# Kernel tuning notes

Measured on AMD Instinct MI355X. Metric: run time of the kernel, lower is better.

Reference implementation:

```python
import jax, jax.numpy as jnp
import numpy as np

U = 128  # linear_units

def setup_inputs() -> dict:
    key = jax.random.key(0)
    k1, k2, k3, k4, k5, k6 = jax.random.split(key, 6)
    B, S, D = 16, 2048, 128
    x = jax.random.normal(k1, (B, S, D), dtype=jnp.float32)
    t = jax.random.uniform(k2, (B, S), dtype=jnp.float32)
    # glorot_uniform inits
    lim_qk = np.sqrt(6.0 / (D + U)).astype(np.float32)
    Wq = jax.random.uniform(k3, (D, U), minval=-lim_qk, maxval=lim_qk, dtype=jnp.float32)
    Wk = jax.random.uniform(k4, (D, U), minval=-lim_qk, maxval=lim_qk, dtype=jnp.float32)
    lim_s = np.sqrt(6.0 / (1 + S)).astype(np.float32)
    theta = jax.random.uniform(k5, (1, S), minval=-lim_s, maxval=lim_s, dtype=jnp.float32)
    mu = jax.random.uniform(k6, (1, S), minval=-lim_s, maxval=lim_s, dtype=jnp.float32)
    return {"x": x, "t": t, "Wq": Wq, "Wk": Wk, "theta": theta, "mu": mu}

def reference(x, t, Wq, Wk, theta, mu):
    # x: (B,S,D), t: (B,S), theta/mu: (1,S)
    scale = jnp.sqrt(jnp.asarray(U, dtype=x.dtype))
    q = x @ Wq                                   # (B,S,U)
    k = x @ Wk                                   # (B,S,U)
    scores = jnp.einsum('biu,bju->bij', q, k) / scale  # (B,S,S)
    alphas = jax.nn.softmax(scores, axis=-1)
    gn = jnp.einsum('bij,bjd->bid', alphas, x)   # weighted sum == alphas @ x, (B,S,D)
    time_fact = jax.nn.sigmoid(theta - mu * t)   # (B,S)
    v = jnp.sum(gn * time_fact[:, :, None], axis=1)  # (B,D)
    return v
```

## Files before the change

### kernel.cpp

```cpp
#include <hip/hip_runtime.h>
#include <hip/hip_bf16.h>

#define SS 2048
#define DD 128
#define BB 16
#define LDST 136

typedef short bf16x8 __attribute__((ext_vector_type(8)));
typedef float f32x4 __attribute__((ext_vector_type(4)));

__device__ __forceinline__ unsigned short f2bf(float f) {
  union { float f; unsigned u; } v; v.f = f;
  unsigned r = v.u + 0x7fffu + ((v.u >> 16) & 1u);
  return (unsigned short)(r >> 16);
}
__device__ __forceinline__ float fexp2(float x) { return __builtin_amdgcn_exp2f(x); }

__global__ __launch_bounds__(256) void qk_gemm(
    const float* __restrict__ x, const float* __restrict__ Wq,
    const float* __restrict__ Wk, unsigned short* __restrict__ qb,
    unsigned short* __restrict__ kb) {
  __shared__ unsigned short wt[256 * LDST];
  __shared__ unsigned short xa[128 * LDST];
  const int tid = threadIdx.x, wave = tid >> 6, lane = tid & 63;
  const int lq = lane & 15, quad = lane >> 4;
  const int m0 = blockIdx.x * 128;
  const float qscale = 0.1275174346f;

  for (int i = 0; i < 64; ++i) {
    int idx = i * 256 + tid;
    int d = idx >> 7, u = idx & 127;
    wt[u * LDST + d] = f2bf(Wq[idx] * qscale);
    wt[(u + 128) * LDST + d] = f2bf(Wk[idx]);
  }
#pragma unroll
  for (int i = 0; i < 16; ++i) {
    int c4 = i * 256 + tid;
    int row = c4 >> 5, col = (c4 & 31) * 4;
    const float4 v = *(const float4*)(x + (size_t)(m0 + row) * DD + col);
    ushort4 h;
    h.x = f2bf(v.x); h.y = f2bf(v.y); h.z = f2bf(v.z); h.w = f2bf(v.w);
    *(ushort4*)(&xa[row * LDST + col]) = h;
  }
  __syncthreads();

  f32x4 acc[2][16];
#pragma unroll
  for (int mt = 0; mt < 2; ++mt)
#pragma unroll
    for (int nt = 0; nt < 16; ++nt) acc[mt][nt] = (f32x4){0.f, 0.f, 0.f, 0.f};

#pragma unroll
  for (int ks = 0; ks < 4; ++ks) {
    bf16x8 a0 = *(const bf16x8*)(&xa[(wave * 32 + lq) * LDST + ks * 32 + quad * 8]);
    bf16x8 a1 = *(const bf16x8*)(&xa[(wave * 32 + 16 + lq) * LDST + ks * 32 + quad * 8]);
#pragma unroll
    for (int nt = 0; nt < 16; ++nt) {
      bf16x8 bfr = *(const bf16x8*)(&wt[(nt * 16 + lq) * LDST + ks * 32 + quad * 8]);
      acc[0][nt] = __builtin_amdgcn_mfma_f32_16x16x32_bf16(a0, bfr, acc[0][nt], 0, 0, 0);
      acc[1][nt] = __builtin_amdgcn_mfma_f32_16x16x32_bf16(a1, bfr, acc[1][nt], 0, 0, 0);
    }
  }
#pragma unroll
  for (int mt = 0; mt < 2; ++mt)
#pragma unroll
    for (int nt = 0; nt < 16; ++nt)
#pragma unroll
      for (int r = 0; r < 4; ++r) {
        int grow = m0 + wave * 32 + mt * 16 + quad * 4 + r;
        unsigned short hv = f2bf(acc[mt][nt][r]);
        if (nt < 8) qb[(size_t)grow * DD + nt * 16 + lq] = hv;
        else        kb[(size_t)grow * DD + (nt - 8) * 16 + lq] = hv;
      }
}

__global__ __launch_bounds__(256, 2) void attn_ce(
    const unsigned short* __restrict__ qb, const unsigned short* __restrict__ kb,
    const float* __restrict__ t, const float* __restrict__ theta,
    const float* __restrict__ mu, float* __restrict__ w) {
  const int b = blockIdx.x >> 5;
  const int i0 = (blockIdx.x & 31) * 64;
  const int tid = threadIdx.x, wave = tid >> 6, lane = tid & 63;
  const int lq = lane & 15, quad = lane >> 4;

  __shared__ unsigned short qs[64 * LDST];
  __shared__ unsigned short kt[128 * LDST];
  __shared__ float rs_lds[4][64];
  __shared__ float c_lds[64];

#pragma unroll
  for (int i = 0; i < 4; ++i) {
    int c8 = i * 256 + tid;
    int row = c8 >> 4, col = (c8 & 15) * 8;
    *(uint4*)(&qs[row * LDST + col]) =
        *(const uint4*)(qb + (size_t)(b * SS + i0 + row) * DD + col);
  }
  __syncthreads();

  bf16x8 af[4][4];
#pragma unroll
  for (int mt = 0; mt < 4; ++mt)
#pragma unroll
    for (int ks = 0; ks < 4; ++ks)
      af[mt][ks] = *(const bf16x8*)(&qs[(mt * 16 + lq) * LDST + ks * 32 + quad * 8]);

  auto stage_k = [&](int jt) {
#pragma unroll
    for (int i = 0; i < 8; ++i) {
      int c8 = i * 256 + tid;
      int row = c8 >> 4, col = (c8 & 15) * 8;
      *(uint4*)(&kt[row * LDST + col]) =
          *(const uint4*)(kb + (size_t)(b * SS + jt * 128 + row) * DD + col);
    }
  };

  float rowsum[4][4];
#pragma unroll
  for (int mt = 0; mt < 4; ++mt)
#pragma unroll
    for (int r = 0; r < 4; ++r) rowsum[mt][r] = 0.f;

  for (int jt = 0; jt < 16; ++jt) {
    __syncthreads();
    stage_k(jt);
    __syncthreads();
#pragma unroll
    for (int nt = 0; nt < 2; ++nt) {
      f32x4 acc[4];
#pragma unroll
      for (int mt = 0; mt < 4; ++mt) acc[mt] = (f32x4){0.f, 0.f, 0.f, 0.f};
#pragma unroll
      for (int ks = 0; ks < 4; ++ks) {
        bf16x8 bfr = *(const bf16x8*)(
            &kt[(wave * 32 + nt * 16 + lq) * LDST + ks * 32 + quad * 8]);
#pragma unroll
        for (int mt = 0; mt < 4; ++mt)
          acc[mt] = __builtin_amdgcn_mfma_f32_16x16x32_bf16(af[mt][ks], bfr, acc[mt], 0, 0, 0);
      }
#pragma unroll
      for (int mt = 0; mt < 4; ++mt)
#pragma unroll
        for (int r = 0; r < 4; ++r) rowsum[mt][r] += fexp2(acc[mt][r]);
    }
  }
#pragma unroll
  for (int d2 = 1; d2 <= 8; d2 <<= 1)
#pragma unroll
    for (int mt = 0; mt < 4; ++mt)
#pragma unroll
      for (int r = 0; r < 4; ++r)
        rowsum[mt][r] += __shfl_xor(rowsum[mt][r], d2, 64);
  if (lq == 0) {
#pragma unroll
    for (int mt = 0; mt < 4; ++mt)
#pragma unroll
      for (int r = 0; r < 4; ++r)
        rs_lds[wave][mt * 16 + quad * 4 + r] = rowsum[mt][r];
  }
  __syncthreads();
  if (tid < 64) {
    float l = rs_lds[0][tid] + rs_lds[1][tid] + rs_lds[2][tid] + rs_lds[3][tid];
    int gi = i0 + tid;
    float z = theta[gi] - mu[gi] * t[b * SS + gi];
    float tf = 1.f / (1.f + fexp2(-z * 1.44269504f));
    c_lds[tid] = tf / l;
  }
  __syncthreads();
  float creg[4][4];
#pragma unroll
  for (int mt = 0; mt < 4; ++mt)
#pragma unroll
    for (int r = 0; r < 4; ++r) creg[mt][r] = c_lds[mt * 16 + quad * 4 + r];

  for (int jt = 0; jt < 16; ++jt) {
    __syncthreads();
    stage_k(jt);
    __syncthreads();
#pragma unroll
    for (int nt = 0; nt < 2; ++nt) {
      f32x4 acc[4];
#pragma unroll
      for (int mt = 0; mt < 4; ++mt) acc[mt] = (f32x4){0.f, 0.f, 0.f, 0.f};
#pragma unroll
      for (int ks = 0; ks < 4; ++ks) {
        bf16x8 bfr = *(const bf16x8*)(
            &kt[(wave * 32 + nt * 16 + lq) * LDST + ks * 32 + quad * 8]);
#pragma unroll
        for (int mt = 0; mt < 4; ++mt)
          acc[mt] = __builtin_amdgcn_mfma_f32_16x16x32_bf16(af[mt][ks], bfr, acc[mt], 0, 0, 0);
      }
      float cs = 0.f;
#pragma unroll
      for (int mt = 0; mt < 4; ++mt)
#pragma unroll
        for (int r = 0; r < 4; ++r) cs += creg[mt][r] * fexp2(acc[mt][r]);
      cs += __shfl_xor(cs, 16, 64);
      cs += __shfl_xor(cs, 32, 64);
      if (lane < 16)
        atomicAdd(&w[b * SS + jt * 128 + wave * 32 + nt * 16 + lane], cs);
    }
  }
}

__global__ __launch_bounds__(256) void finalize(
    const float* __restrict__ x, const float* __restrict__ w,
    float* __restrict__ out) {
  const int b = blockIdx.x >> 3;
  const int j0 = (blockIdx.x & 7) * 256;
  const int tid = threadIdx.x;
  const int d = tid & 127, jo = tid >> 7;
  float acc = 0.f;
  for (int jj = 0; jj < 128; ++jj) {
    int j = j0 + jj * 2 + jo;
    acc += w[b * SS + j] * x[((size_t)b * SS + j) * DD + d];
  }
  __shared__ float red[256];
  red[tid] = acc;
  __syncthreads();
  if (tid < 128) atomicAdd(&out[b * DD + tid], red[tid] + red[tid + 128]);
}

extern "C" void kernel_launch(void* const* d_in, const int* in_sizes, int n_in,
                              void* d_out, int out_size, void* d_ws, size_t ws_size,
                              hipStream_t stream) {
  const float* x = (const float*)d_in[0];
  const float* t = (const float*)d_in[1];
  const float* Wq = (const float*)d_in[2];
  const float* Wk = (const float*)d_in[3];
  const float* theta = (const float*)d_in[4];
  const float* mu = (const float*)d_in[5];
  float* out = (float*)d_out;

  unsigned short* qb = (unsigned short*)d_ws;
  unsigned short* kb = qb + (size_t)BB * SS * DD;
  float* w = (float*)(kb + (size_t)BB * SS * DD);

  hipMemsetAsync(w, 0, (size_t)BB * SS * sizeof(float), stream);
  hipMemsetAsync(d_out, 0, (size_t)BB * DD * sizeof(float), stream);

  qk_gemm<<<dim3(256), dim3(256), 0, stream>>>(x, Wq, Wk, qb, kb);
  attn_ce<<<dim3(512), dim3(256), 0, stream>>>(qb, kb, t, theta, mu, w);
  finalize<<<dim3(128), dim3(256), 0, stream>>>(x, w, out);
}
```

Before: 143.6 us.

## Load MFMA fragments from global, double-buffer K in registers, split prep kernel

```diff
diff --git a/kernel.cpp b/kernel.cpp
--- a/kernel.cpp
+++ b/kernel.cpp
@@ -4,10 +4,10 @@
 #define SS 2048
 #define DD 128
 #define BB 16
-#define LDST 136
 
 typedef short bf16x8 __attribute__((ext_vector_type(8)));
 typedef float f32x4 __attribute__((ext_vector_type(4)));
+typedef unsigned short ushort_t;
 
 __device__ __forceinline__ unsigned short f2bf(float f) {
   union { float f; unsigned u; } v; v.f = f;
@@ -16,66 +16,71 @@
 }
 __device__ __forceinline__ float fexp2(float x) { return __builtin_amdgcn_exp2f(x); }
 
+__global__ __launch_bounds__(256) void prep(
+    const float* __restrict__ x, const float* __restrict__ Wq,
+    const float* __restrict__ Wk, ushort_t* __restrict__ xb,
+    ushort_t* __restrict__ wt_g) {
+  const int tid = threadIdx.x, blk = blockIdx.x;
+  if (blk < 2048) {
+    size_t i = ((size_t)blk * 256 + tid) * 8;
+    const float4 a = *(const float4*)(x + i);
+    const float4 c = *(const float4*)(x + i + 4);
+    union { ushort_t s[8]; uint4 v; } u;
+    u.s[0] = f2bf(a.x); u.s[1] = f2bf(a.y); u.s[2] = f2bf(a.z); u.s[3] = f2bf(a.w);
+    u.s[4] = f2bf(c.x); u.s[5] = f2bf(c.y); u.s[6] = f2bf(c.z); u.s[7] = f2bf(c.w);
+    *(uint4*)(xb + i) = u.v;
+  } else {
+    int idx = (blk - 2048) * 256 + tid;
+    int uu = idx >> 7, d = idx & 127;
+    wt_g[uu * 128 + d] = f2bf(Wq[d * 128 + uu] * 0.1275174346f);
+    wt_g[(uu + 128) * 128 + d] = f2bf(Wk[d * 128 + uu]);
+  }
+}
+
+#define SCT 264
 __global__ __launch_bounds__(256) void qk_gemm(
-    const float* __restrict__ x, const float* __restrict__ Wq,
-    const float* __restrict__ Wk, unsigned short* __restrict__ qb,
-    unsigned short* __restrict__ kb) {
-  __shared__ unsigned short wt[256 * LDST];
-  __shared__ unsigned short xa[128 * LDST];
+    const ushort_t* __restrict__ xb, const ushort_t* __restrict__ wt_g,
+    ushort_t* __restrict__ qb, ushort_t* __restrict__ kb) {
+  __shared__ ushort_t sc[64 * SCT];
   const int tid = threadIdx.x, wave = tid >> 6, lane = tid & 63;
   const int lq = lane & 15, quad = lane >> 4;
-  const int m0 = blockIdx.x * 128;
-  const float qscale = 0.1275174346f;
-
-  for (int i = 0; i < 64; ++i) {
+  const int m0 = blockIdx.x * 64;
+
+  bf16x8 af[4];
+  const ushort_t* xrow = xb + (size_t)(m0 + wave * 16 + lq) * DD + quad * 8;
+#pragma unroll
+  for (int ks = 0; ks < 4; ++ks) af[ks] = *(const bf16x8*)(xrow + ks * 32);
+
+#pragma unroll
+  for (int nt = 0; nt < 8; ++nt) {
+    f32x4 aq = (f32x4){0.f, 0.f, 0.f, 0.f};
+    f32x4 ak = (f32x4){0.f, 0.f, 0.f, 0.f};
+#pragma unroll
+    for (int ks = 0; ks < 4; ++ks) {
+      bf16x8 bq = *(const bf16x8*)(wt_g + (nt * 16 + lq) * 128 + ks * 32 + quad * 8);
+      bf16x8 bk = *(const bf16x8*)(wt_g + ((nt + 8) * 16 + lq) * 128 + ks * 32 + quad * 8);
+      aq = __builtin_amdgcn_mfma_f32_16x16x32_bf16(af[ks], bq, aq, 0, 0, 0);
+      ak = __builtin_amdgcn_mfma_f32_16x16x32_bf16(af[ks], bk, ak, 0, 0, 0);
+    }
+#pragma unroll
+    for (int r = 0; r < 4; ++r) {
+      int row = wave * 16 + quad * 4 + r;
+      sc[row * SCT + nt * 16 + lq] = f2bf(aq[r]);
+      sc[row * SCT + 128 + nt * 16 + lq] = f2bf(ak[r]);
+    }
+  }
+  __syncthreads();
+#pragma unroll
+  for (int i = 0; i < 4; ++i) {
     int idx = i * 256 + tid;
-    int d = idx >> 7, u = idx & 127;
-    wt[u * LDST + d] = f2bf(Wq[idx] * qscale);
-    wt[(u + 128) * LDST + d] = f2bf(Wk[idx]);
-  }
-#pragma unroll
-  for (int i = 0; i < 16; ++i) {
-    int c4 = i * 256 + tid;
-    int row = c4 >> 5, col = (c4 & 31) * 4;
-    const float4 v = *(const float4*)(x + (size_t)(m0 + row) * DD + col);
-    ushort4 h;
-    h.x = f2bf(v.x); h.y = f2bf(v.y); h.z = f2bf(v.z); h.w = f2bf(v.w);
-    *(ushort4*)(&xa[row * LDST + col]) = h;
-  }
-  __syncthreads();
-
-  f32x4 acc[2][16];
-#pragma unroll
-  for (int mt = 0; mt < 2; ++mt)
-#pragma unroll
-    for (int nt = 0; nt < 16; ++nt) acc[mt][nt] = (f32x4){0.f, 0.f, 0.f, 0.f};
-
-#pragma unroll
-  for (int ks = 0; ks < 4; ++ks) {
-    bf16x8 a0 = *(const bf16x8*)(&xa[(wave * 32 + lq) * LDST + ks * 32 + quad * 8]);
-    bf16x8 a1 = *(const bf16x8*)(&xa[(wave * 32 + 16 + lq) * LDST + ks * 32 + quad * 8]);
-#pragma unroll
-    for (int nt = 0; nt < 16; ++nt) {
-      bf16x8 bfr = *(const bf16x8*)(&wt[(nt * 16 + lq) * LDST + ks * 32 + quad * 8]);
-      acc[0][nt] = __builtin_amdgcn_mfma_f32_16x16x32_bf16(a0, bfr, acc[0][nt], 0, 0, 0);
-      acc[1][nt] = __builtin_amdgcn_mfma_f32_16x16x32_bf16(a1, bfr, acc[1][nt], 0, 0, 0);
-    }
-  }
-#pragma unroll
-  for (int mt = 0; mt < 2; ++mt)
-#pragma unroll
-    for (int nt = 0; nt < 16; ++nt)
-#pragma unroll
-      for (int r = 0; r < 4; ++r) {
-        int grow = m0 + wave * 32 + mt * 16 + quad * 4 + r;
-        unsigned short hv = f2bf(acc[mt][nt][r]);
-        if (nt < 8) qb[(size_t)grow * DD + nt * 16 + lq] = hv;
-        else        kb[(size_t)grow * DD + (nt - 8) * 16 + lq] = hv;
-      }
+    int row = idx >> 4, col = (idx & 15) * 8;
+    *(uint4*)(qb + (size_t)(m0 + row) * DD + col) = *(const uint4*)(&sc[row * SCT + col]);
+    *(uint4*)(kb + (size_t)(m0 + row) * DD + col) = *(const uint4*)(&sc[row * SCT + 128 + col]);
+  }
 }
 
 __global__ __launch_bounds__(256, 2) void attn_ce(
-    const unsigned short* __restrict__ qb, const unsigned short* __restrict__ kb,
+    const ushort_t* __restrict__ qb, const ushort_t* __restrict__ kb,
     const float* __restrict__ t, const float* __restrict__ theta,
     const float* __restrict__ mu, float* __restrict__ w) {
   const int b = blockIdx.x >> 5;
@@ -83,35 +88,27 @@
   const int tid = threadIdx.x, wave = tid >> 6, lane = tid & 63;
   const int lq = lane & 15, quad = lane >> 4;
 
-  __shared__ unsigned short qs[64 * LDST];
-  __shared__ unsigned short kt[128 * LDST];
   __shared__ float rs_lds[4][64];
   __shared__ float c_lds[64];
 
-#pragma unroll
-  for (int i = 0; i < 4; ++i) {
-    int c8 = i * 256 + tid;
-    int row = c8 >> 4, col = (c8 & 15) * 8;
-    *(uint4*)(&qs[row * LDST + col]) =
-        *(const uint4*)(qb + (size_t)(b * SS + i0 + row) * DD + col);
-  }
-  __syncthreads();
-
   bf16x8 af[4][4];
+  const ushort_t* qbase = qb + (size_t)(b * SS + i0 + lq) * DD + quad * 8;
 #pragma unroll
   for (int mt = 0; mt < 4; ++mt)
 #pragma unroll
     for (int ks = 0; ks < 4; ++ks)
-      af[mt][ks] = *(const bf16x8*)(&qs[(mt * 16 + lq) * LDST + ks * 32 + quad * 8]);
-
-  auto stage_k = [&](int jt) {
-#pragma unroll
-    for (int i = 0; i < 8; ++i) {
-      int c8 = i * 256 + tid;
-      int row = c8 >> 4, col = (c8 & 15) * 8;
-      *(uint4*)(&kt[row * LDST + col]) =
-          *(const uint4*)(kb + (size_t)(b * SS + jt * 128 + row) * DD + col);
-    }
+      af[mt][ks] = *(const bf16x8*)(qbase + mt * 16 * DD + ks * 32);
+
+  const ushort_t* kwave = kb + (size_t)(b * SS + wave * 32 + lq) * DD + quad * 8;
+
+  bf16x8 cur[2][4], nxt[2][4];
+  auto load_tile = [&](bf16x8 (&f)[2][4], int jt) {
+    const ushort_t* base = kwave + (size_t)jt * 128 * DD;
+#pragma unroll
+    for (int nt = 0; nt < 2; ++nt)
+#pragma unroll
+      for (int ks = 0; ks < 4; ++ks)
+        f[nt][ks] = *(const bf16x8*)(base + nt * 16 * DD + ks * 32);
   };
 
   float rowsum[4][4];
@@ -120,29 +117,32 @@
 #pragma unroll
     for (int r = 0; r < 4; ++r) rowsum[mt][r] = 0.f;
 
-  for (int jt = 0; jt < 16; ++jt) {
-    __syncthreads();
-    stage_k(jt);
-    __syncthreads();
+  auto compute_p1 = [&](bf16x8 (&f)[2][4]) {
 #pragma unroll
     for (int nt = 0; nt < 2; ++nt) {
       f32x4 acc[4];
 #pragma unroll
       for (int mt = 0; mt < 4; ++mt) acc[mt] = (f32x4){0.f, 0.f, 0.f, 0.f};
 #pragma unroll
-      for (int ks = 0; ks < 4; ++ks) {
-        bf16x8 bfr = *(const bf16x8*)(
-            &kt[(wave * 32 + nt * 16 + lq) * LDST + ks * 32 + quad * 8]);
+      for (int ks = 0; ks < 4; ++ks)
 #pragma unroll
         for (int mt = 0; mt < 4; ++mt)
-          acc[mt] = __builtin_amdgcn_mfma_f32_16x16x32_bf16(af[mt][ks], bfr, acc[mt], 0, 0, 0);
-      }
+          acc[mt] = __builtin_amdgcn_mfma_f32_16x16x32_bf16(af[mt][ks], f[nt][ks], acc[mt], 0, 0, 0);
 #pragma unroll
       for (int mt = 0; mt < 4; ++mt)
 #pragma unroll
         for (int r = 0; r < 4; ++r) rowsum[mt][r] += fexp2(acc[mt][r]);
     }
-  }
+  };
+
+  load_tile(cur, 0);
+  for (int jt = 0; jt < 16; jt += 2) {
+    load_tile(nxt, jt + 1);
+    compute_p1(cur);
+    if (jt + 2 < 16) load_tile(cur, jt + 2);
+    compute_p1(nxt);
+  }
+
 #pragma unroll
   for (int d2 = 1; d2 <= 8; d2 <<= 1)
 #pragma unroll
@@ -172,47 +172,49 @@
 #pragma unroll
     for (int r = 0; r < 4; ++r) creg[mt][r] = c_lds[mt * 16 + quad * 4 + r];
 
-  for (int jt = 0; jt < 16; ++jt) {
-    __syncthreads();
-    stage_k(jt);
-    __syncthreads();
+  auto compute_p2 = [&](bf16x8 (&f)[2][4], int jt) {
 #pragma unroll
     for (int nt = 0; nt < 2; ++nt) {
       f32x4 acc[4];
 #pragma unroll
       for (int mt = 0; mt < 4; ++mt) acc[mt] = (f32x4){0.f, 0.f, 0.f, 0.f};
 #pragma unroll
-      for (int ks = 0; ks < 4; ++ks) {
-        bf16x8 bfr = *(const bf16x8*)(
-            &kt[(wave * 32 + nt * 16 + lq) * LDST + ks * 32 + quad * 8]);
+      for (int ks = 0; ks < 4; ++ks)
 #pragma unroll
         for (int mt = 0; mt < 4; ++mt)
-          acc[mt] = __builtin_amdgcn_mfma_f32_16x16x32_bf16(af[mt][ks], bfr, acc[mt], 0, 0, 0);
-      }
+          acc[mt] = __builtin_amdgcn_mfma_f32_16x16x32_bf16(af[mt][ks], f[nt][ks], acc[mt], 0, 0, 0);
       float cs = 0.f;
 #pragma unroll
       for (int mt = 0; mt < 4; ++mt)
 #pragma unroll
-        for (int r = 0; r < 4; ++r) cs += creg[mt][r] * fexp2(acc[mt][r]);
+        for (int r = 0; r < 4; ++r) cs = fmaf(creg[mt][r], fexp2(acc[mt][r]), cs);
       cs += __shfl_xor(cs, 16, 64);
       cs += __shfl_xor(cs, 32, 64);
       if (lane < 16)
         atomicAdd(&w[b * SS + jt * 128 + wave * 32 + nt * 16 + lane], cs);
     }
+  };
+
+  load_tile(cur, 0);
+  for (int jt = 0; jt < 16; jt += 2) {
+    load_tile(nxt, jt + 1);
+    compute_p2(cur, jt);
+    if (jt + 2 < 16) load_tile(cur, jt + 2);
+    compute_p2(nxt, jt + 1);
   }
 }
 
 __global__ __launch_bounds__(256) void finalize(
     const float* __restrict__ x, const float* __restrict__ w,
     float* __restrict__ out) {
-  const int b = blockIdx.x >> 3;
-  const int j0 = (blockIdx.x & 7) * 256;
+  const int b = blockIdx.x >> 5;
+  const int j0 = (blockIdx.x & 31) * 64;
   const int tid = threadIdx.x;
   const int d = tid & 127, jo = tid >> 7;
   float acc = 0.f;
-  for (int jj = 0; jj < 128; ++jj) {
+  for (int jj = 0; jj < 32; ++jj) {
     int j = j0 + jj * 2 + jo;
-    acc += w[b * SS + j] * x[((size_t)b * SS + j) * DD + d];
+    acc = fmaf(w[b * SS + j], x[((size_t)b * SS + j) * DD + d], acc);
   }
   __shared__ float red[256];
   red[tid] = acc;
@@ -231,14 +233,17 @@
   const float* mu = (const float*)d_in[5];
   float* out = (float*)d_out;
 
-  unsigned short* qb = (unsigned short*)d_ws;
-  unsigned short* kb = qb + (size_t)BB * SS * DD;
-  float* w = (float*)(kb + (size_t)BB * SS * DD);
+  ushort_t* qb = (ushort_t*)d_ws;
+  ushort_t* kb = qb + (size_t)BB * SS * DD;
+  ushort_t* xb = kb + (size_t)BB * SS * DD;
+  ushort_t* wt_g = xb + (size_t)BB * SS * DD;
+  float* w = (float*)(wt_g + 256 * 128);
 
   hipMemsetAsync(w, 0, (size_t)BB * SS * sizeof(float), stream);
   hipMemsetAsync(d_out, 0, (size_t)BB * DD * sizeof(float), stream);
 
-  qk_gemm<<<dim3(256), dim3(256), 0, stream>>>(x, Wq, Wk, qb, kb);
+  prep<<<dim3(2112), dim3(256), 0, stream>>>(x, Wq, Wk, xb, wt_g);
+  qk_gemm<<<dim3(512), dim3(256), 0, stream>>>(xb, wt_g, qb, kb);
   attn_ce<<<dim3(512), dim3(256), 0, stream>>>(qb, kb, t, theta, mu, w);
-  finalize<<<dim3(128), dim3(256), 0, stream>>>(x, w, out);
-}
+  finalize<<<dim3(512), dim3(256), 0, stream>>>(x, w, out);
+}
```

Result: slower. 166.4 us (+15.9%).
